# Performance work log

Hardware: AMD Instinct MI355X
Metric: run time of the kernel (lower is better)

Reference implementation:

```python
import jax, jax.numpy as jnp
import numpy as np

EPS = 1e-5

def conv2d(x, w, b, pad):
    # x: [B,C,H,W], w: [O,I,kh,kw] (OIHW), b: [O]
    y = jax.lax.conv_general_dilated(x, w, (1, 1), [(pad, pad), (pad, pad)],
                                     dimension_numbers=('NCHW', 'OIHW', 'NCHW'))
    return y + b[None, :, None, None]

def bn(x, g, b, m, v):
    # eval-mode BatchNorm2d
    scale = (g / jnp.sqrt(v + EPS))[None, :, None, None]
    return (x - m[None, :, None, None]) * scale + b[None, :, None, None]


def setup_inputs() -> dict:
    key = jax.random.key(0)
    ks = jax.random.split(key, 16)
    B, C, H, W = 2, 64, 64, 64
    Cq = C // 8
    f = lambda k, shp, s=0.05: jax.random.normal(k, shp, dtype=jnp.float32) * s
    return {
        'x': jax.random.normal(ks[0], (B, C, H, W), dtype=jnp.float32),
        'sW': f(ks[1], (C, C, 3, 3)), 'sb': f(ks[2], (C,)),
        's_g': jnp.ones((C,), jnp.float32), 's_b': jnp.zeros((C,), jnp.float32),
        's_m': jnp.zeros((C,), jnp.float32), 's_v': jnp.ones((C,), jnp.float32),
        'cW': f(ks[3], (C, C, 3, 3)), 'cb': f(ks[4], (C,)),
        'c_g': jnp.ones((C,), jnp.float32), 'c_b': jnp.zeros((C,), jnp.float32),
        'c_m': jnp.zeros((C,), jnp.float32), 'c_v': jnp.ones((C,), jnp.float32),
        'qW': f(ks[5], (Cq, C, 1, 1)), 'qb': f(ks[6], (Cq,)),
        'kW': f(ks[7], (Cq, C, 1, 1)), 'kb': f(ks[8], (Cq,)),
        'vW': f(ks[9], (C, C, 1, 1)), 'vb': f(ks[10], (C,)),
        'oW': f(ks[11], (C, C, 1, 1)), 'ob': f(ks[12], (C,)),
        's_gamma': jnp.array([0.5], jnp.float32),
        'c_gamma': jnp.array([0.5], jnp.float32),
    }


def reference(x, sW, sb, s_g, s_b, s_m, s_v, cW, cb, c_g, c_b, c_m, c_v,
              qW, qb, kW, kb, vW, vb, oW, ob, s_gamma, c_gamma):
    # ---- spatial attention branch ----
    s_x = jax.nn.relu(bn(conv2d(x, sW, sb, 1), s_g, s_b, s_m, s_v))  # [B,C,H,W]
    B, C, H, W = s_x.shape
    HW = H * W
    q = conv2d(x, qW, qb, 0).reshape(B, -1, HW)  # [B, C/8, HW]
    k = conv2d(x, kW, kb, 0).reshape(B, -1, HW)  # [B, C/8, HW]
    v = conv2d(x, vW, vb, 0).reshape(B, C, HW)   # [B, C,   HW]
    # aff[b,i,j] = q_i . k_j ; softmax over j (unscaled, per original)
    A = jax.nn.softmax(jnp.einsum('bdi,bdj->bij', q, k), axis=-1)  # [B,HW,HW]
    sa = jnp.einsum('bcj,bij->bci', v, A).reshape(B, C, H, W)
    sa_map = s_gamma[0] * sa + s_x
    # ---- channel attention branch ----
    c_x = jax.nn.relu(bn(conv2d(x, cW, cb, 1), c_g, c_b, c_m, c_v))  # [B,C,H,W]
    fmap = c_x.reshape(B, C, HW)
    Ac = jnp.einsum('bin,bjn->bij', fmap, fmap)  # [B,C,C]
    Ac = jax.nn.softmax(jnp.max(Ac, axis=-1, keepdims=True) - Ac, axis=-1)
    ca = jnp.einsum('bij,bjn->bin', Ac, fmap).reshape(B, C, H, W)
    ca_map = c_gamma[0] * ca + c_x
    # ---- fuse + output adaptor ----
    return conv2d(sa_map + ca_map, oW, ob, 0)
```

## Files before the change

### kernel.cpp

```cpp
#include <hip/hip_runtime.h>

#define HW 4096

typedef __attribute__((ext_vector_type(8)))  short short8;
typedef __attribute__((ext_vector_type(16))) float float16;

__device__ __forceinline__ unsigned short f2bf(float f) {
    unsigned u = __float_as_uint(f);
    u += 0x7fffu + ((u >> 16) & 1u);
    return (unsigned short)(u >> 16);
}

__global__ __launch_bounds__(256) void k_wprep(
    const float* __restrict__ sW, const float* __restrict__ cW,
    const float* __restrict__ sb, const float* __restrict__ cb,
    const float* __restrict__ s_g, const float* __restrict__ s_b,
    const float* __restrict__ s_m, const float* __restrict__ s_v,
    const float* __restrict__ c_g, const float* __restrict__ c_b,
    const float* __restrict__ c_m, const float* __restrict__ c_v,
    unsigned short* __restrict__ Wa, float* __restrict__ scsh)
{
    int bx = blockIdx.x;
    int which = bx / 9, khw = bx % 9;
    const float* W = which ? cW : sW;
    int t = threadIdx.x;
#pragma unroll
    for (int i = 0; i < 16; i++) {
        int idx = t + 256 * i;
        int oc = idx >> 6, ic = idx & 63;
        float v = W[(size_t)(oc * 64 + ic) * 9 + khw];
        Wa[((size_t)(which * 9 + khw) * 64 + oc) * 64 + ic] = f2bf(v);
    }
    if (bx == 0 && t < 128) {
        int wh = t >> 6, oc = t & 63;
        const float* g  = wh ? c_g : s_g;
        const float* bb = wh ? c_b : s_b;
        const float* m  = wh ? c_m : s_m;
        const float* vv = wh ? c_v : s_v;
        const float* cbias = wh ? cb : sb;
        float scale = g[oc] * rsqrtf(vv[oc] + 1e-5f);
        scsh[wh * 128 + oc]      = scale;
        scsh[wh * 128 + 64 + oc] = (cbias[oc] - m[oc]) * scale + bb[oc];
    }
}

__global__ __launch_bounds__(256) void k_conv_qkv(
    const float* __restrict__ x, const unsigned short* __restrict__ Wa,
    const float* __restrict__ scsh,
    const float* __restrict__ qW, const float* __restrict__ qb,
    const float* __restrict__ kW, const float* __restrict__ kb,
    const float* __restrict__ vW, const float* __restrict__ vb,
    float* __restrict__ sx, float* __restrict__ cx,
    unsigned short* __restrict__ qT, unsigned short* __restrict__ kT,
    unsigned short* __restrict__ vB)
{
    __shared__ unsigned short xs[3 * 8 * 66 * 8];
    int bx = blockIdx.x;
    int t = threadIdx.x;

    if (bx < 256) {
        int which = bx >> 7;
        int b     = (bx >> 6) & 1;
        int row   = bx & 63;

        const float* xb = x + (size_t)(b * 64) * HW;
#pragma unroll
        for (int it = 0; it < 24; it++) {
            int idx = t + 256 * it;
            int lr  = idx >> 11;
            int rem = idx & 2047;
            int icp = rem >> 6;
            int col = rem & 63;
            int ir  = row - 1 + lr;
            unsigned pack = 0;
            if (ir >= 0 && ir < 64) {
                float v0 = xb[(size_t)(icp * 2)     * HW + ir * 64 + col];
                float v1 = xb[(size_t)(icp * 2 + 1) * HW + ir * 64 + col];
                pack = (unsigned)f2bf(v0) | ((unsigned)f2bf(v1) << 16);
            }
            int icg = icp >> 2, io = icp & 3;
            *(unsigned*)&xs[(((lr * 8 + icg) * 66 + col + 1) * 8) + io * 2] = pack;
        }
        if (t < 192) {
            int pair = t & 3;
            int colsel = (t >> 2) & 1;
            int rg = t >> 3;
            *(unsigned*)&xs[((rg * 66 + colsel * 65) * 8) + pair * 2] = 0u;
        }
        __syncthreads();

        int lane = t & 63, w = t >> 6;
        int l31 = lane & 31, half = lane >> 5;
        int colh = w & 1;
        int m0   = (w >> 1) * 32;
        int c    = colh * 32 + l31;

        float16 acc;
#pragma unroll
        for (int i = 0; i < 16; i++) acc[i] = 0.f;

        const unsigned short* Wbase =
            Wa + ((size_t)which * 9) * 4096 + (size_t)(m0 + l31) * 64 + half * 8;

#pragma unroll
        for (int khw = 0; khw < 9; khw++) {
            const int kh = khw / 3, kw = khw % 3;
#pragma unroll
            for (int icq = 0; icq < 4; icq++) {
                short8 af = *(const short8*)(Wbase + (size_t)khw * 4096 + icq * 16);
                const unsigned short* bp =
                    &xs[((kh * 8 + icq * 2 + half) * 66 + kw) * 8];
                short8 bf = *(const short8*)(bp + (size_t)c * 8);
                acc = __builtin_amdgcn_mfma_f32_32x32x16_bf16(af, bf, acc, 0, 0, 0);
            }
        }

        float* out = (which ? cx : sx) + (size_t)(b * 64) * HW;
        const float* sc = scsh + which * 128;
        int hwbase = row * 64 + c;
#pragma unroll
        for (int r = 0; r < 16; r++) {
            int oc = m0 + (r & 3) + 8 * (r >> 2) + 4 * half;
            float s  = sc[oc];
            float sh = sc[64 + oc];
            out[(size_t)oc * HW + hwbase] = fmaxf(acc[r] * s + sh, 0.f);
        }
    } else {
        int qbx = bx - 256;
        int b = qbx / 80, rem = qbx % 80;
        int chunk = rem / 5, g = rem % 5;
        int hw = chunk * 256 + t;
        const float* xb = x + (size_t)(b * 64) * HW + hw;

        float acc[16];
#pragma unroll
        for (int u = 0; u < 16; u++) acc[u] = 0.f;

        if (g == 0) {
            for (int ic = 0; ic < 64; ic++) {
                float xv = xb[ic * HW];
#pragma unroll
                for (int u = 0; u < 8; u++) acc[u]     += qW[u * 64 + ic] * xv;
#pragma unroll
                for (int u = 0; u < 8; u++) acc[8 + u] += kW[u * 64 + ic] * xv;
            }
            short8 qv, kv;
#pragma unroll
            for (int u = 0; u < 8; u++) qv[u] = (short)f2bf(acc[u] + qb[u]);
#pragma unroll
            for (int u = 0; u < 8; u++) kv[u] = (short)f2bf(acc[8 + u] + kb[u]);
            *(short8*)(qT + ((size_t)(b * HW) + hw) * 8) = qv;
            *(short8*)(kT + ((size_t)(b * HW) + hw) * 8) = kv;
        } else {
            int c0 = (g - 1) * 16;
            for (int ic = 0; ic < 64; ic++) {
                float xv = xb[ic * HW];
#pragma unroll
                for (int u = 0; u < 16; u++) acc[u] += vW[(c0 + u) * 64 + ic] * xv;
            }
            int m  = hw & 15;
            int sg = (m & 3) | ((m & 4) << 1) | ((m & 8) >> 1);
            size_t base = ((size_t)(b * 256) + (hw >> 4)) * 1024 + sg;
#pragma unroll
            for (int u = 0; u < 16; u++)
                vB[base + (size_t)(c0 + u) * 16] = f2bf(acc[u] + vb[c0 + u]);
        }
    }
}

union SmemKB {
    struct { float o_sh[4][64][33]; float den_sh[4][32]; } a;
    float slab[32][68];
};

__global__ __launch_bounds__(256) void k_attn_gram(
    const unsigned short* __restrict__ qT, const unsigned short* __restrict__ kT,
    const unsigned short* __restrict__ vB, const float* __restrict__ cx,
    float* __restrict__ Opart, float* __restrict__ denp,
    float* __restrict__ Gpart)
{
    __shared__ SmemKB sm;
    int bx = blockIdx.x;
    int t = threadIdx.x;

    if (bx < 512) {
        int lane = t & 63, w = t >> 6;
        int half = lane >> 5, l31 = lane & 31;
        int b  = bx >> 8;
        int itile = (bx >> 1) & 127;
        int jh = bx & 1;
        int i0 = itile * 32;

        short8 qf;
        if (half == 0) {
            qf = *(const short8*)(qT + ((size_t)(b * HW) + i0 + l31) * 8);
        } else {
#pragma unroll
            for (int i = 0; i < 8; i++) qf[i] = 0;
        }

        float16 o0, o1;
#pragma unroll
        for (int i = 0; i < 16; i++) { o0[i] = 0.f; o1[i] = 0.f; }
        float denr = 0.f;

        const unsigned short* kTb = kT + (size_t)(b * HW) * 8;
        const unsigned short* vBb = vB + (size_t)b * (256 * 1024);

        for (int tile = 0; tile < 16; tile++) {
            int j0 = jh * 2048 + w * 512 + tile * 32;
            int g0 = j0 >> 4;

            short8 kf;
            if (half == 0) {
                kf = *(const short8*)(kTb + (size_t)(j0 + l31) * 8);
            } else {
#pragma unroll
                for (int i = 0; i < 8; i++) kf[i] = 0;
            }

            float16 z;
#pragma unroll
            for (int i = 0; i < 16; i++) z[i] = 0.f;
            float16 s = __builtin_amdgcn_mfma_f32_32x32x16_bf16(kf, qf, z, 0, 0, 0);

            float p[16];
#pragma unroll
            for (int r = 0; r < 16; r++) {
                p[r] = __expf(s[r]);
                denr += p[r];
            }
            short8 pa0, pa1;
#pragma unroll
            for (int r = 0; r < 8; r++) {
                pa0[r] = (short)f2bf(p[r]);
                pa1[r] = (short)f2bf(p[8 + r]);
            }

            const unsigned short* vg0 = vBb + (size_t)g0 * 1024 + half * 8;
            short8 v00 = *(const short8*)(vg0 + (size_t)l31 * 16);
            short8 v01 = *(const short8*)(vg0 + (size_t)(32 + l31) * 16);
            short8 v10 = *(const short8*)(vg0 + 1024 + (size_t)l31 * 16);
            short8 v11 = *(const short8*)(vg0 + 1024 + (size_t)(32 + l31) * 16);

            o0 = __builtin_amdgcn_mfma_f32_32x32x16_bf16(pa0, v00, o0, 0, 0, 0);
            o1 = __builtin_amdgcn_mfma_f32_32x32x16_bf16(pa0, v01, o1, 0, 0, 0);
            o0 = __builtin_amdgcn_mfma_f32_32x32x16_bf16(pa1, v10, o0, 0, 0, 0);
            o1 = __builtin_amdgcn_mfma_f32_32x32x16_bf16(pa1, v11, o1, 0, 0, 0);
        }

        float dfull = denr + __shfl_xor(denr, 32);
        if (half == 0) sm.a.den_sh[w][l31] = dfull;
#pragma unroll
        for (int r = 0; r < 16; r++) {
            int il = (r & 3) + 8 * (r >> 2) + 4 * half;
            sm.a.o_sh[w][l31][il]      = o0[r];
            sm.a.o_sh[w][32 + l31][il] = o1[r];
        }
        __syncthreads();

        int i  = t & 31;
        int cg = t >> 5;
        if (cg == 0)
            denp[jh * 8192 + b * 4096 + i0 + i] =
                sm.a.den_sh[0][i] + sm.a.den_sh[1][i] +
                sm.a.den_sh[2][i] + sm.a.den_sh[3][i];
#pragma unroll
        for (int u = 0; u < 8; u++) {
            int c = cg * 8 + u;
            float sv = sm.a.o_sh[0][c][i] + sm.a.o_sh[1][c][i]
                     + sm.a.o_sh[2][c][i] + sm.a.o_sh[3][c][i];
            Opart[((size_t)(jh * 2 + b) * 64 + c) * HW + i0 + i] = sv;
        }
    } else {
        int gbx = bx - 512;
        int b = gbx >> 7, slice = gbx & 127;
        int hw0 = slice * 32;

#pragma unroll
        for (int it = 0; it < 2; it++) {
            int idx = t + 256 * it;
            int hw = idx & 31, c0 = (idx >> 5) * 4;
            float4 vv;
            vv.x = cx[(size_t)(b * 64 + c0 + 0) * HW + hw0 + hw];
            vv.y = cx[(size_t)(b * 64 + c0 + 1) * HW + hw0 + hw];
            vv.z = cx[(size_t)(b * 64 + c0 + 2) * HW + hw0 + hw];
            vv.w = cx[(size_t)(b * 64 + c0 + 3) * HW + hw0 + hw];
            *(float4*)&sm.slab[hw][c0] = vv;
        }
        __syncthreads();

        int i0 = (t & 15) * 4, j0 = (t >> 4) * 4;
        float acc[4][4] = {};
#pragma unroll 8
        for (int hw = 0; hw < 32; hw++) {
            float4 ai = *(const float4*)&sm.slab[hw][i0];
            float4 aj = *(const float4*)&sm.slab[hw][j0];
            acc[0][0] += ai.x * aj.x; acc[0][1] += ai.x * aj.y;
            acc[0][2] += ai.x * aj.z; acc[0][3] += ai.x * aj.w;
            acc[1][0] += ai.y * aj.x; acc[1][1] += ai.y * aj.y;
            acc[1][2] += ai.y * aj.z; acc[1][3] += ai.y * aj.w;
            acc[2][0] += ai.z * aj.x; acc[2][1] += ai.z * aj.y;
            acc[2][2] += ai.z * aj.z; acc[2][3] += ai.z * aj.w;
            acc[3][0] += ai.w * aj.x; acc[3][1] += ai.w * aj.y;
            acc[3][2] += ai.w * aj.z; acc[3][3] += ai.w * aj.w;
        }

        float* Gb = Gpart + ((size_t)(b * 128 + slice) * 64) * 64;
#pragma unroll
        for (int ii = 0; ii < 4; ii++)
            *(float4*)&Gb[(size_t)(i0 + ii) * 64 + j0] =
                make_float4(acc[ii][0], acc[ii][1], acc[ii][2], acc[ii][3]);
    }
}

__global__ __launch_bounds__(64) void k_csoft(
    const float* __restrict__ Gpart, float* __restrict__ AcsT)
{
    int row = blockIdx.x;
    int b = row >> 6, i = row & 63;
    int j = threadIdx.x;

    const float* Gp = Gpart + ((size_t)(b * 128) * 64 + i) * 64 + j;
    float a = 0.f;
#pragma unroll 4
    for (int sl = 0; sl < 128; sl++)
        a += Gp[(size_t)sl * 4096];

    float mn = a;
    mn = fminf(mn, __shfl_xor(mn, 1));
    mn = fminf(mn, __shfl_xor(mn, 2));
    mn = fminf(mn, __shfl_xor(mn, 4));
    mn = fminf(mn, __shfl_xor(mn, 8));
    mn = fminf(mn, __shfl_xor(mn, 16));
    mn = fminf(mn, __shfl_xor(mn, 32));
    float p = __expf(mn - a);
    float s = p;
    s += __shfl_xor(s, 1);
    s += __shfl_xor(s, 2);
    s += __shfl_xor(s, 4);
    s += __shfl_xor(s, 8);
    s += __shfl_xor(s, 16);
    s += __shfl_xor(s, 32);
    AcsT[(size_t)b * 4096 + j * 64 + i] = p / s;
}

__global__ __launch_bounds__(256) void k_fuse_out(
    const float* __restrict__ Opart, const float* __restrict__ denp,
    const float* __restrict__ sx,    const float* __restrict__ cx,
    const float* __restrict__ AcsT,
    const float* __restrict__ oW,    const float* __restrict__ ob,
    const float* __restrict__ s_gamma, const float* __restrict__ c_gamma,
    float* __restrict__ out)
{
    __shared__ float A_sh[64][68];
    __shared__ float cxs[64][33];
    __shared__ float f_sh[64][33];
    __shared__ float oWT[64][68];

    int bx = blockIdx.x;
    int b = bx >> 7, chunk = bx & 127;
    int px0 = chunk * 32;
    int t = threadIdx.x;
    float sgam = s_gamma[0], cgam = c_gamma[0];

#pragma unroll
    for (int k = 0; k < 16; k++) {
        int idx = t + 256 * k;
        int j = idx >> 6, i = idx & 63;
        A_sh[j][i] = AcsT[(size_t)b * 4096 + idx];
        oWT[j][i]  = oW[(size_t)i * 64 + j];
    }
#pragma unroll
    for (int k = 0; k < 8; k++) {
        int idx = t + 256 * k;
        int c = idx >> 5, px = idx & 31;
        size_t o = (size_t)(b * 64 + c) * HW + px0 + px;
        float cv = cx[o];
        cxs[c][px] = cv;
        float d = denp[b * 4096 + px0 + px] + denp[8192 + b * 4096 + px0 + px];
        float O = Opart[((size_t)(b)*64 + c) * HW + px0 + px]
                + Opart[((size_t)(2 + b) * 64 + c) * HW + px0 + px];
        f_sh[c][px] = sgam * (O / d) + sx[o] + cv;
    }
    __syncthreads();

    {
        int px = t & 31, cg = t >> 5;
        int c0 = cg * 8;
        float ca[8] = {};
        for (int j = 0; j < 64; j++) {
            float xv = cxs[j][px];
            float4 a0 = *(const float4*)&A_sh[j][c0];
            float4 a1 = *(const float4*)&A_sh[j][c0 + 4];
            ca[0] += a0.x * xv; ca[1] += a0.y * xv;
            ca[2] += a0.z * xv; ca[3] += a0.w * xv;
            ca[4] += a1.x * xv; ca[5] += a1.y * xv;
            ca[6] += a1.z * xv; ca[7] += a1.w * xv;
        }
#pragma unroll
        for (int u = 0; u < 8; u++)
            f_sh[c0 + u][px] += cgam * ca[u];
    }
    __syncthreads();

    {
        int px = t & 31, og = t >> 5;
        int o0 = og * 8;
        float acc[8] = {};
        for (int c = 0; c < 64; c++) {
            float fv = f_sh[c][px];
            float4 a0 = *(const float4*)&oWT[c][o0];
            float4 a1 = *(const float4*)&oWT[c][o0 + 4];
            acc[0] += a0.x * fv; acc[1] += a0.y * fv;
            acc[2] += a0.z * fv; acc[3] += a0.w * fv;
            acc[4] += a1.x * fv; acc[5] += a1.y * fv;
            acc[6] += a1.z * fv; acc[7] += a1.w * fv;
        }
#pragma unroll
        for (int u = 0; u < 8; u++) {
            int o = o0 + u;
            out[(size_t)(b * 64 + o) * HW + px0 + px] = acc[u] + ob[o];
        }
    }
}

extern "C" void kernel_launch(void* const* d_in, const int* in_sizes, int n_in,
                              void* d_out, int out_size, void* d_ws, size_t ws_size,
                              hipStream_t stream)
{
    const float* x    = (const float*)d_in[0];
    const float* sW   = (const float*)d_in[1];
    const float* sb   = (const float*)d_in[2];
    const float* s_g  = (const float*)d_in[3];
    const float* s_b  = (const float*)d_in[4];
    const float* s_m  = (const float*)d_in[5];
    const float* s_v  = (const float*)d_in[6];
    const float* cW   = (const float*)d_in[7];
    const float* cb   = (const float*)d_in[8];
    const float* c_g  = (const float*)d_in[9];
    const float* c_b  = (const float*)d_in[10];
    const float* c_m  = (const float*)d_in[11];
    const float* c_v  = (const float*)d_in[12];
    const float* qW   = (const float*)d_in[13];
    const float* qb   = (const float*)d_in[14];
    const float* kW   = (const float*)d_in[15];
    const float* kb   = (const float*)d_in[16];
    const float* vW   = (const float*)d_in[17];
    const float* vb   = (const float*)d_in[18];
    const float* oW   = (const float*)d_in[19];
    const float* ob   = (const float*)d_in[20];
    const float* s_gamma = (const float*)d_in[21];
    const float* c_gamma = (const float*)d_in[22];

    float* ws    = (float*)d_ws;
    float* sx    = ws;
    float* cx    = ws + 524288;
    float* Opart = ws + 1048576;
    float* denp  = ws + 2097152;
    float* AcsT  = ws + 2113536;
    float* Gpart = ws + 2121728;
    float* scsh  = ws + 3170304;
    unsigned short* us = (unsigned short*)(ws + 3170560);
    unsigned short* qT = us;
    unsigned short* kT = us + 65536;
    unsigned short* vB = us + 131072;
    unsigned short* Wa = us + 655360;

    k_wprep<<<18, 256, 0, stream>>>(sW, cW, sb, cb, s_g, s_b, s_m, s_v,
                                    c_g, c_b, c_m, c_v, Wa, scsh);
    k_conv_qkv<<<416, 256, 0, stream>>>(x, Wa, scsh, qW, qb, kW, kb, vW, vb,
                                        sx, cx, qT, kT, vB);
    k_attn_gram<<<768, 256, 0, stream>>>(qT, kT, vB, cx, Opart, denp, Gpart);
    k_csoft<<<128, 64, 0, stream>>>(Gpart, AcsT);
    k_fuse_out<<<256, 256, 0, stream>>>(Opart, denp, sx, cx, AcsT,
                                        oW, ob, s_gamma, c_gamma, (float*)d_out);
}
```

Before: 170.9 us.

## Split attention j-range four ways, vectorize conv staging, coarsen Gram slices

The spatial attention kernel now splits the key dimension into four parts instead of two, doubling block count, and the fuse kernel sums four partial outputs and denominators. Conv input staging uses float4 loads, and the Gram partials cover 128 pixels per block (32 slices), so the channel-softmax reduction reads fewer partials. The transposed output weight is precomputed once in the prep kernel, and launch-bounds occupancy hints are added. The cost is more partial-sum traffic for the attention output and extra workspace.

```diff
diff --git a/kernel.cpp b/kernel.cpp
--- a/kernel.cpp
+++ b/kernel.cpp
@@ -18,33 +18,44 @@
     const float* __restrict__ s_m, const float* __restrict__ s_v,
     const float* __restrict__ c_g, const float* __restrict__ c_b,
     const float* __restrict__ c_m, const float* __restrict__ c_v,
-    unsigned short* __restrict__ Wa, float* __restrict__ scsh)
+    const float* __restrict__ oW,
+    unsigned short* __restrict__ Wa, float* __restrict__ scsh,
+    float* __restrict__ oWTg)
 {
     int bx = blockIdx.x;
-    int which = bx / 9, khw = bx % 9;
-    const float* W = which ? cW : sW;
     int t = threadIdx.x;
-#pragma unroll
-    for (int i = 0; i < 16; i++) {
-        int idx = t + 256 * i;
-        int oc = idx >> 6, ic = idx & 63;
-        float v = W[(size_t)(oc * 64 + ic) * 9 + khw];
-        Wa[((size_t)(which * 9 + khw) * 64 + oc) * 64 + ic] = f2bf(v);
-    }
-    if (bx == 0 && t < 128) {
-        int wh = t >> 6, oc = t & 63;
-        const float* g  = wh ? c_g : s_g;
-        const float* bb = wh ? c_b : s_b;
-        const float* m  = wh ? c_m : s_m;
-        const float* vv = wh ? c_v : s_v;
-        const float* cbias = wh ? cb : sb;
-        float scale = g[oc] * rsqrtf(vv[oc] + 1e-5f);
-        scsh[wh * 128 + oc]      = scale;
-        scsh[wh * 128 + 64 + oc] = (cbias[oc] - m[oc]) * scale + bb[oc];
-    }
-}
-
-__global__ __launch_bounds__(256) void k_conv_qkv(
+    if (bx < 18) {
+        int which = bx / 9, khw = bx % 9;
+        const float* W = which ? cW : sW;
+#pragma unroll
+        for (int i = 0; i < 16; i++) {
+            int idx = t + 256 * i;
+            int oc = idx >> 6, ic = idx & 63;
+            float v = W[(size_t)(oc * 64 + ic) * 9 + khw];
+            Wa[((size_t)(which * 9 + khw) * 64 + oc) * 64 + ic] = f2bf(v);
+        }
+        if (bx == 0 && t < 128) {
+            int wh = t >> 6, oc = t & 63;
+            const float* g  = wh ? c_g : s_g;
+            const float* bb = wh ? c_b : s_b;
+            const float* m  = wh ? c_m : s_m;
+            const float* vv = wh ? c_v : s_v;
+            const float* cbias = wh ? cb : sb;
+            float scale = g[oc] * rsqrtf(vv[oc] + 1e-5f);
+            scsh[wh * 128 + oc]      = scale;
+            scsh[wh * 128 + 64 + oc] = (cbias[oc] - m[oc]) * scale + bb[oc];
+        }
+    } else {
+#pragma unroll
+        for (int k = 0; k < 16; k++) {
+            int idx = t + 256 * k;
+            int c = idx >> 6, o = idx & 63;
+            oWTg[idx] = oW[(size_t)o * 64 + c];
+        }
+    }
+}
+
+__global__ __launch_bounds__(256, 3) void k_conv_qkv(
     const float* __restrict__ x, const unsigned short* __restrict__ Wa,
     const float* __restrict__ scsh,
     const float* __restrict__ qW, const float* __restrict__ qb,
@@ -62,24 +73,30 @@
         int which = bx >> 7;
         int b     = (bx >> 6) & 1;
         int row   = bx & 63;
-
         const float* xb = x + (size_t)(b * 64) * HW;
-#pragma unroll
-        for (int it = 0; it < 24; it++) {
-            int idx = t + 256 * it;
-            int lr  = idx >> 11;
-            int rem = idx & 2047;
-            int icp = rem >> 6;
-            int col = rem & 63;
-            int ir  = row - 1 + lr;
-            unsigned pack = 0;
+
+#pragma unroll
+        for (int it = 0; it < 6; it++) {
+            int idx  = t + 256 * it;
+            int col4 = idx & 15;
+            int icp  = (idx >> 4) & 31;
+            int lr   = idx >> 9;
+            int ir   = row - 1 + lr;
+            float fa[4] = {0.f, 0.f, 0.f, 0.f};
+            float fb[4] = {0.f, 0.f, 0.f, 0.f};
             if (ir >= 0 && ir < 64) {
-                float v0 = xb[(size_t)(icp * 2)     * HW + ir * 64 + col];
-                float v1 = xb[(size_t)(icp * 2 + 1) * HW + ir * 64 + col];
-                pack = (unsigned)f2bf(v0) | ((unsigned)f2bf(v1) << 16);
+                const float* p0 = xb + (size_t)(icp * 2) * HW + ir * 64 + col4 * 4;
+                float4 v0 = *(const float4*)p0;
+                float4 v1 = *(const float4*)(p0 + HW);
+                fa[0] = v0.x; fa[1] = v0.y; fa[2] = v0.z; fa[3] = v0.w;
+                fb[0] = v1.x; fb[1] = v1.y; fb[2] = v1.z; fb[3] = v1.w;
             }
             int icg = icp >> 2, io = icp & 3;
-            *(unsigned*)&xs[(((lr * 8 + icg) * 66 + col + 1) * 8) + io * 2] = pack;
+#pragma unroll
+            for (int j = 0; j < 4; j++) {
+                unsigned pack = (unsigned)f2bf(fa[j]) | ((unsigned)f2bf(fb[j]) << 16);
+                *(unsigned*)&xs[(((lr * 8 + icg) * 66 + col4 * 4 + j + 1) * 8) + io * 2] = pack;
+            }
         }
         if (t < 192) {
             int pair = t & 3;
@@ -126,8 +143,8 @@
             out[(size_t)oc * HW + hwbase] = fmaxf(acc[r] * s + sh, 0.f);
         }
     } else {
-        int qbx = bx - 256;
-        int b = qbx / 80, rem = qbx % 80;
+        int ubx = bx - 256;
+        int b = ubx / 80, rem = ubx % 80;
         int chunk = rem / 5, g = rem % 5;
         int hw = chunk * 256 + t;
         const float* xb = x + (size_t)(b * 64) * HW + hw;
@@ -170,10 +187,10 @@
 
 union SmemKB {
     struct { float o_sh[4][64][33]; float den_sh[4][32]; } a;
-    float slab[32][68];
+    float slab[64][68];
 };
 
-__global__ __launch_bounds__(256) void k_attn_gram(
+__global__ __launch_bounds__(256, 4) void k_attn_gram(
     const unsigned short* __restrict__ qT, const unsigned short* __restrict__ kT,
     const unsigned short* __restrict__ vB, const float* __restrict__ cx,
     float* __restrict__ Opart, float* __restrict__ denp,
@@ -183,12 +200,12 @@
     int bx = blockIdx.x;
     int t = threadIdx.x;
 
-    if (bx < 512) {
+    if (bx < 1024) {
         int lane = t & 63, w = t >> 6;
         int half = lane >> 5, l31 = lane & 31;
-        int b  = bx >> 8;
-        int itile = (bx >> 1) & 127;
-        int jh = bx & 1;
+        int b  = bx >> 9;
+        int itile = (bx >> 2) & 127;
+        int jh = bx & 3;
         int i0 = itile * 32;
 
         short8 qf;
@@ -207,8 +224,8 @@
         const unsigned short* kTb = kT + (size_t)(b * HW) * 8;
         const unsigned short* vBb = vB + (size_t)b * (256 * 1024);
 
-        for (int tile = 0; tile < 16; tile++) {
-            int j0 = jh * 2048 + w * 512 + tile * 32;
+        for (int tile = 0; tile < 8; tile++) {
+            int j0 = jh * 1024 + w * 256 + tile * 32;
             int g0 = j0 >> 4;
 
             short8 kf;
@@ -224,17 +241,17 @@
             for (int i = 0; i < 16; i++) z[i] = 0.f;
             float16 s = __builtin_amdgcn_mfma_f32_32x32x16_bf16(kf, qf, z, 0, 0, 0);
 
-            float p[16];
+            float pr[16];
 #pragma unroll
             for (int r = 0; r < 16; r++) {
-                p[r] = __expf(s[r]);
-                denr += p[r];
+                pr[r] = __expf(s[r]);
+                denr += pr[r];
             }
             short8 pa0, pa1;
 #pragma unroll
             for (int r = 0; r < 8; r++) {
-                pa0[r] = (short)f2bf(p[r]);
-                pa1[r] = (short)f2bf(p[8 + r]);
+                pa0[r] = (short)f2bf(pr[r]);
+                pa1[r] = (short)f2bf(pr[8 + r]);
             }
 
             const unsigned short* vg0 = vBb + (size_t)g0 * 1024 + half * 8;
@@ -273,58 +290,54 @@
             Opart[((size_t)(jh * 2 + b) * 64 + c) * HW + i0 + i] = sv;
         }
     } else {
-        int gbx = bx - 512;
-        int b = gbx >> 7, slice = gbx & 127;
-        int hw0 = slice * 32;
-
-#pragma unroll
-        for (int it = 0; it < 2; it++) {
-            int idx = t + 256 * it;
-            int hw = idx & 31, c0 = (idx >> 5) * 4;
-            float4 vv;
-            vv.x = cx[(size_t)(b * 64 + c0 + 0) * HW + hw0 + hw];
-            vv.y = cx[(size_t)(b * 64 + c0 + 1) * HW + hw0 + hw];
-            vv.z = cx[(size_t)(b * 64 + c0 + 2) * HW + hw0 + hw];
-            vv.w = cx[(size_t)(b * 64 + c0 + 3) * HW + hw0 + hw];
-            *(float4*)&sm.slab[hw][c0] = vv;
-        }
-        __syncthreads();
-
-        int i0 = (t & 15) * 4, j0 = (t >> 4) * 4;
+        int gbx = bx - 1024;
+        int b = gbx >> 5, slice = gbx & 31;
+        int i0 = (t & 15) * 4, j0c = (t >> 4) * 4;
         float acc[4][4] = {};
+#pragma unroll
+        for (int ch = 0; ch < 2; ch++) {
+            int hwb = slice * 128 + ch * 64;
+            __syncthreads();
+#pragma unroll
+            for (int it = 0; it < 16; it++) {
+                int idx = t + 256 * it;
+                int hw = idx & 63, c = idx >> 6;
+                sm.slab[hw][c] = cx[(size_t)(b * 64 + c) * HW + hwb + hw];
+            }
+            __syncthreads();
 #pragma unroll 8
-        for (int hw = 0; hw < 32; hw++) {
-            float4 ai = *(const float4*)&sm.slab[hw][i0];
-            float4 aj = *(const float4*)&sm.slab[hw][j0];
-            acc[0][0] += ai.x * aj.x; acc[0][1] += ai.x * aj.y;
-            acc[0][2] += ai.x * aj.z; acc[0][3] += ai.x * aj.w;
-            acc[1][0] += ai.y * aj.x; acc[1][1] += ai.y * aj.y;
-            acc[1][2] += ai.y * aj.z; acc[1][3] += ai.y * aj.w;
-            acc[2][0] += ai.z * aj.x; acc[2][1] += ai.z * aj.y;
-            acc[2][2] += ai.z * aj.z; acc[2][3] += ai.z * aj.w;
-            acc[3][0] += ai.w * aj.x; acc[3][1] += ai.w * aj.y;
-            acc[3][2] += ai.w * aj.z; acc[3][3] += ai.w * aj.w;
-        }
-
-        float* Gb = Gpart + ((size_t)(b * 128 + slice) * 64) * 64;
+            for (int hw = 0; hw < 64; hw++) {
+                float4 ai = *(const float4*)&sm.slab[hw][i0];
+                float4 aj = *(const float4*)&sm.slab[hw][j0c];
+                acc[0][0] += ai.x * aj.x; acc[0][1] += ai.x * aj.y;
+                acc[0][2] += ai.x * aj.z; acc[0][3] += ai.x * aj.w;
+                acc[1][0] += ai.y * aj.x; acc[1][1] += ai.y * aj.y;
+                acc[1][2] += ai.y * aj.z; acc[1][3] += ai.y * aj.w;
+                acc[2][0] += ai.z * aj.x; acc[2][1] += ai.z * aj.y;
+                acc[2][2] += ai.z * aj.z; acc[2][3] += ai.z * aj.w;
+                acc[3][0] += ai.w * aj.x; acc[3][1] += ai.w * aj.y;
+                acc[3][2] += ai.w * aj.z; acc[3][3] += ai.w * aj.w;
+            }
+        }
+        float* Gb = Gpart + ((size_t)(b * 32 + slice)) * 4096;
 #pragma unroll
         for (int ii = 0; ii < 4; ii++)
-            *(float4*)&Gb[(size_t)(i0 + ii) * 64 + j0] =
+            *(float4*)&Gb[(size_t)(i0 + ii) * 64 + j0c] =
                 make_float4(acc[ii][0], acc[ii][1], acc[ii][2], acc[ii][3]);
     }
 }
 
-__global__ __launch_bounds__(64) void k_csoft(
+__global__ __launch_bounds__(256) void k_csoft(
     const float* __restrict__ Gpart, float* __restrict__ AcsT)
 {
-    int row = blockIdx.x;
-    int b = row >> 6, i = row & 63;
-    int j = threadIdx.x;
-
-    const float* Gp = Gpart + ((size_t)(b * 128) * 64 + i) * 64 + j;
+    int r = blockIdx.x * 4 + (threadIdx.x >> 6);
+    int b = r >> 6, i = r & 63;
+    int j = threadIdx.x & 63;
+
+    const float* Gp = Gpart + (size_t)(b * 32) * 4096 + i * 64 + j;
     float a = 0.f;
-#pragma unroll 4
-    for (int sl = 0; sl < 128; sl++)
+#pragma unroll 8
+    for (int sl = 0; sl < 32; sl++)
         a += Gp[(size_t)sl * 4096];
 
     float mn = a;
@@ -349,7 +362,7 @@
     const float* __restrict__ Opart, const float* __restrict__ denp,
     const float* __restrict__ sx,    const float* __restrict__ cx,
     const float* __restrict__ AcsT,
-    const float* __restrict__ oW,    const float* __restrict__ ob,
+    const float* __restrict__ oWTg,  const float* __restrict__ ob,
     const float* __restrict__ s_gamma, const float* __restrict__ c_gamma,
     float* __restrict__ out)
 {
@@ -369,7 +382,7 @@
         int idx = t + 256 * k;
         int j = idx >> 6, i = idx & 63;
         A_sh[j][i] = AcsT[(size_t)b * 4096 + idx];
-        oWT[j][i]  = oW[(size_t)i * 64 + j];
+        oWT[j][i]  = oWTg[idx];
     }
 #pragma unroll
     for (int k = 0; k < 8; k++) {
@@ -378,10 +391,15 @@
         size_t o = (size_t)(b * 64 + c) * HW + px0 + px;
         float cv = cx[o];
         cxs[c][px] = cv;
-        float d = denp[b * 4096 + px0 + px] + denp[8192 + b * 4096 + px0 + px];
-        float O = Opart[((size_t)(b)*64 + c) * HW + px0 + px]
-                + Opart[((size_t)(2 + b) * 64 + c) * HW + px0 + px];
-        f_sh[c][px] = sgam * (O / d) + sx[o] + cv;
+        float dd = denp[b * 4096 + px0 + px]
+                 + denp[8192  + b * 4096 + px0 + px]
+                 + denp[16384 + b * 4096 + px0 + px]
+                 + denp[24576 + b * 4096 + px0 + px];
+        float O = Opart[((size_t)(0 + b) * 64 + c) * HW + px0 + px]
+                + Opart[((size_t)(2 + b) * 64 + c) * HW + px0 + px]
+                + Opart[((size_t)(4 + b) * 64 + c) * HW + px0 + px]
+                + Opart[((size_t)(6 + b) * 64 + c) * HW + px0 + px];
+        f_sh[c][px] = sgam * (O / dd) + sx[o] + cv;
     }
     __syncthreads();
 
@@ -457,22 +475,23 @@
     float* sx    = ws;
     float* cx    = ws + 524288;
     float* Opart = ws + 1048576;
-    float* denp  = ws + 2097152;
-    float* AcsT  = ws + 2113536;
-    float* Gpart = ws + 2121728;
-    float* scsh  = ws + 3170304;
-    unsigned short* us = (unsigned short*)(ws + 3170560);
+    float* denp  = ws + 3145728;
+    float* AcsT  = ws + 3178496;
+    float* Gpart = ws + 3186688;
+    float* oWTg  = ws + 3448832;
+    float* scsh  = ws + 3452928;
+    unsigned short* us = (unsigned short*)(ws + 3453184);
     unsigned short* qT = us;
     unsigned short* kT = us + 65536;
     unsigned short* vB = us + 131072;
     unsigned short* Wa = us + 655360;
 
-    k_wprep<<<18, 256, 0, stream>>>(sW, cW, sb, cb, s_g, s_b, s_m, s_v,
-                                    c_g, c_b, c_m, c_v, Wa, scsh);
+    k_wprep<<<19, 256, 0, stream>>>(sW, cW, sb, cb, s_g, s_b, s_m, s_v,
+                                    c_g, c_b, c_m, c_v, oW, Wa, scsh, oWTg);
     k_conv_qkv<<<416, 256, 0, stream>>>(x, Wa, scsh, qW, qb, kW, kb, vW, vb,
                                         sx, cx, qT, kT, vB);
-    k_attn_gram<<<768, 256, 0, stream>>>(qT, kT, vB, cx, Opart, denp, Gpart);
-    k_csoft<<<128, 64, 0, stream>>>(Gpart, AcsT);
+    k_attn_gram<<<1088, 256, 0, stream>>>(qT, kT, vB, cx, Opart, denp, Gpart);
+    k_csoft<<<32, 256, 0, stream>>>(Gpart, AcsT);
     k_fuse_out<<<256, 256, 0, stream>>>(Opart, denp, sx, cx, AcsT,
-                                        oW, ob, s_gamma, c_gamma, (float*)d_out);
-}
+                                        oWTg, ob, s_gamma, c_gamma, (float*)d_out);
+}
```

Result: faster. 160.8 us, median of 2 (-5.9%).
